# Optimization experiments

Measured on AMD Instinct MI355X. Metric: run time of the kernel, lower is better.

## Reference

```python
import jax, jax.numpy as jnp
import numpy as np

N, M, FIN, FOUT, K = 16, 65536, 32, 32, 7


def setup_inputs() -> dict:
    key = jax.random.key(0)
    k1, k2, k3, k4, k5 = jax.random.split(key, 5)
    stdv = 1.0 / np.sqrt(FIN)
    x = jax.random.normal(k1, (N, M, FIN), dtype=jnp.float32)
    weight = jax.random.uniform(k2, (K, FIN, FOUT), dtype=jnp.float32, minval=-stdv, maxval=stdv)
    bias = jax.random.uniform(k3, (FOUT,), dtype=jnp.float32, minval=-stdv, maxval=stdv)
    index_list = jax.random.randint(k4, (M * K,), 0, M, dtype=jnp.int32)
    index_value = jax.random.uniform(k5, (M, K), dtype=jnp.float32)
    return {"x": x, "weight": weight, "bias": bias,
            "index_list": index_list, "index_value": index_value}


def reference(x, weight, bias, index_list, index_value):
    # out[n,m,o] = sum_k sum_f index_value[m,k] * x[n, idx[m,k], f] * weight[k,f,o] + bias[o]
    n, m, fin = x.shape
    k = index_value.shape[1]
    idx = index_list.reshape(m, k)            # [M, K] neighbor ids
    gathered = x[:, idx, :]                    # [N, M, K, Fin] gather of neighbor feats
    weighted = gathered * index_value[None, :, :, None]  # apply adjacency weights
    out = jnp.einsum('nmkf,kfo->nmo', weighted, weight) + bias
    return out
```

## Files before the change

kernel.cpp:

```cpp
#include <hip/hip_runtime.h>
#include <hip/hip_bf16.h>

#define N_    16
#define M_    65536
#define FIN_  32
#define FOUT_ 32
#define K_    7

#define TOTAL_WAVES_ 8192
#define ITERS_       (M_ / TOTAL_WAVES_)

typedef __bf16 bf16x8 __attribute__((ext_vector_type(8)));
typedef float  f32x4  __attribute__((ext_vector_type(4)));

__global__ __launch_bounds__(256)
void transpose_kernel(const float* __restrict__ x, __bf16* __restrict__ xT)
{
    const int tid = blockIdx.x * blockDim.x + threadIdx.x;
    const int f8 = tid & 3;
    const int n  = (tid >> 2) & 15;
    const int m  = tid >> 6;

    const float4* src = (const float4*)(x + ((size_t)n * M_ + m) * FIN_ + f8 * 8);
    const float4 v0 = src[0];
    const float4 v1 = src[1];
    const float av[8] = {v0.x, v0.y, v0.z, v0.w, v1.x, v1.y, v1.z, v1.w};

    bf16x8 b;
    #pragma unroll
    for (int j = 0; j < 8; ++j) b[j] = (__bf16)av[j];

    *(bf16x8*)(xT + ((size_t)m * N_ + n) * FIN_ + f8 * 8) = b;
}

__global__ __launch_bounds__(256, 4)
void gfc_bf16_kernel(const __bf16* __restrict__ xT,
                     const float* __restrict__ w,
                     const float* __restrict__ bias,
                     const int*   __restrict__ index_list,
                     const float* __restrict__ index_value,
                     float* __restrict__ out)
{
    const int lane  = threadIdx.x & 63;
    const int col   = lane & 15;
    const int kgrp  = lane >> 4;

    const int waves_per_block = blockDim.x >> 6;
    const int wave_id = blockIdx.x * waves_per_block + (threadIdx.x >> 6);

    bf16x8 bfrag[K_][2];
    #pragma unroll
    for (int k = 0; k < K_; ++k) {
        #pragma unroll
        for (int h = 0; h < 2; ++h) {
            const float* wp = w + (size_t)k * (FIN_ * FOUT_)
                                + (size_t)(kgrp * 8) * FOUT_ + h * 16 + col;
            bf16x8 b;
            #pragma unroll
            for (int j = 0; j < 8; ++j)
                b[j] = (__bf16)wp[j * FOUT_];
            bfrag[k][h] = b;
        }
    }
    const float b_lo = bias[col];
    const float b_hi = bias[16 + col];

    const size_t lane_elt = (size_t)col * FIN_ + kgrp * 8;

    int m = __builtin_amdgcn_readfirstlane(wave_id);

    int   idxs[K_];
    float ivs[K_];
    #pragma unroll
    for (int k = 0; k < K_; ++k) {
        idxs[k] = index_list[m * K_ + k];
        ivs[k]  = index_value[m * K_ + k];
    }
    bf16x8 raw[K_];
    #pragma unroll
    for (int k = 0; k < K_; ++k)
        raw[k] = *(const bf16x8*)(xT + (size_t)idxs[k] * (N_ * FIN_) + lane_elt);

    for (int i = 0; i < ITERS_; ++i) {
        const bool has_next = (i + 1) < ITERS_;
        const int  m_next   = __builtin_amdgcn_readfirstlane(m + TOTAL_WAVES_);

        int   idxn[K_];
        float ivn[K_];
        if (has_next) {
            #pragma unroll
            for (int k = 0; k < K_; ++k) {
                idxn[k] = index_list[m_next * K_ + k];
                ivn[k]  = index_value[m_next * K_ + k];
            }
        }

        f32x4 acc0 = {0.f, 0.f, 0.f, 0.f};
        f32x4 acc1 = {0.f, 0.f, 0.f, 0.f};
        #pragma unroll
        for (int k = 0; k < K_; ++k) {
            const float ivk = ivs[k];
            bf16x8 a;
            #pragma unroll
            for (int j = 0; j < 8; ++j)
                a[j] = (__bf16)((float)raw[k][j] * ivk);
            acc0 = __builtin_amdgcn_mfma_f32_16x16x32_bf16(a, bfrag[k][0], acc0, 0, 0, 0);
            acc1 = __builtin_amdgcn_mfma_f32_16x16x32_bf16(a, bfrag[k][1], acc1, 0, 0, 0);
        }

        if (has_next) {
            #pragma unroll
            for (int k = 0; k < K_; ++k)
                raw[k] = *(const bf16x8*)(xT + (size_t)idxn[k] * (N_ * FIN_) + lane_elt);
            #pragma unroll
            for (int k = 0; k < K_; ++k) {
                idxs[k] = idxn[k];
                ivs[k]  = ivn[k];
            }
        }

        #pragma unroll
        for (int r = 0; r < 4; ++r) {
            const int n = kgrp * 4 + r;
            float* op = out + ((size_t)n * M_ + (size_t)m) * FOUT_;
            __builtin_nontemporal_store(acc0[r] + b_lo, op + col);
            __builtin_nontemporal_store(acc1[r] + b_hi, op + 16 + col);
        }

        m = m_next;
    }
}

__global__ __launch_bounds__(256, 4)
void gfc_fallback_kernel(const float* __restrict__ x,
                         const float* __restrict__ w,
                         const float* __restrict__ bias,
                         const int*   __restrict__ index_list,
                         const float* __restrict__ index_value,
                         float* __restrict__ out)
{
    const int lane  = threadIdx.x & 63;
    const int col   = lane & 15;
    const int kgrp  = lane >> 4;

    const int waves_per_block = blockDim.x >> 6;
    const int wave_id     = blockIdx.x * waves_per_block + (threadIdx.x >> 6);
    const int total_waves = gridDim.x * waves_per_block;

    bf16x8 bfrag[K_][2];
    #pragma unroll
    for (int k = 0; k < K_; ++k) {
        #pragma unroll
        for (int h = 0; h < 2; ++h) {
            const float* wp = w + (size_t)k * (FIN_ * FOUT_)
                                + (size_t)(kgrp * 8) * FOUT_ + h * 16 + col;
            bf16x8 b;
            #pragma unroll
            for (int j = 0; j < 8; ++j)
                b[j] = (__bf16)wp[j * FOUT_];
            bfrag[k][h] = b;
        }
    }
    const float b_lo = bias[col];
    const float b_hi = bias[16 + col];

    for (int m = wave_id; m < M_; m += total_waves) {
        f32x4 acc0 = {0.f, 0.f, 0.f, 0.f};
        f32x4 acc1 = {0.f, 0.f, 0.f, 0.f};

        #pragma unroll
        for (int k = 0; k < K_; ++k) {
            const int   m2  = index_list[m * K_ + k];
            const float ivk = index_value[m * K_ + k];
            const float* ap = x + ((size_t)col * M_ + (size_t)m2) * FIN_ + kgrp * 8;
            const float4 v0 = *(const float4*)(ap);
            const float4 v1 = *(const float4*)(ap + 4);
            const float av[8] = {v0.x, v0.y, v0.z, v0.w, v1.x, v1.y, v1.z, v1.w};
            bf16x8 a;
            #pragma unroll
            for (int j = 0; j < 8; ++j)
                a[j] = (__bf16)(av[j] * ivk);
            acc0 = __builtin_amdgcn_mfma_f32_16x16x32_bf16(a, bfrag[k][0], acc0, 0, 0, 0);
            acc1 = __builtin_amdgcn_mfma_f32_16x16x32_bf16(a, bfrag[k][1], acc1, 0, 0, 0);
        }

        #pragma unroll
        for (int r = 0; r < 4; ++r) {
            const int n = kgrp * 4 + r;
            const size_t base = ((size_t)n * M_ + (size_t)m) * FOUT_;
            out[base + col]      = acc0[r] + b_lo;
            out[base + 16 + col] = acc1[r] + b_hi;
        }
    }
}

extern "C" void kernel_launch(void* const* d_in, const int* in_sizes, int n_in,
                              void* d_out, int out_size, void* d_ws, size_t ws_size,
                              hipStream_t stream) {
    const float* x    = (const float*)d_in[0];
    const float* w    = (const float*)d_in[1];
    const float* bias = (const float*)d_in[2];
    const int*   il   = (const int*)  d_in[3];
    const float* iv   = (const float*)d_in[4];
    float* out = (float*)d_out;

    const size_t ws_needed = (size_t)M_ * N_ * FIN_ * sizeof(__bf16);
    if (ws_size >= ws_needed) {
        __bf16* xT = (__bf16*)d_ws;
        const int t_total = N_ * M_ * FIN_ / 8;
        hipLaunchKernelGGL(transpose_kernel, dim3(t_total / 256), dim3(256), 0, stream,
                           x, xT);
        hipLaunchKernelGGL(gfc_bf16_kernel, dim3(2048), dim3(256), 0, stream,
                           xT, w, bias, il, iv, out);
    } else {
        hipLaunchKernelGGL(gfc_fallback_kernel, dim3(2048), dim3(256), 0, stream,
                           x, w, bias, il, iv, out);
    }
}
```

Baseline: 311.2 us.

## Partition batch across XCDs so each die's L2 holds its own bf16 slice

Drops the [M,N,FIN] transpose and writes x as plain bf16 in its original [N,M,FIN] layout. The main kernel is remapped so each XCD (blockIdx & 7) handles only two batch slices, and each MFMA row is now one of 16 consecutive m values rather than one of 16 n values. The per-XCD gather working set therefore fits in that XCD's L2, and the convert kernel becomes a straight streaming copy. Weight fragments move from registers into LDS to cut register pressure, at the cost of per-k LDS reads and more scattered index loads per lane.

Measured after the change: 340.6 us. +9.4%, slower.

```diff
diff --git a/kernel.cpp b/kernel.cpp
--- a/kernel.cpp
+++ b/kernel.cpp
@@ -7,91 +7,97 @@
 #define FOUT_ 32
 #define K_    7
 
-#define TOTAL_WAVES_ 8192
-#define ITERS_       (M_ / TOTAL_WAVES_)
+#define BLOCKS_   2048
+#define THREADS_  256
+#define WAVES_PB_ 4
+#define NXCD_     8
+#define WAVES_PER_XCD_ ((BLOCKS_ / NXCD_) * WAVES_PB_)
+#define GROUPS_   (M_ / 16)
+#define ITERS_    8
 
 typedef __bf16 bf16x8 __attribute__((ext_vector_type(8)));
 typedef float  f32x4  __attribute__((ext_vector_type(4)));
 
 __global__ __launch_bounds__(256)
-void transpose_kernel(const float* __restrict__ x, __bf16* __restrict__ xT)
+void convert_kernel(const float* __restrict__ x, __bf16* __restrict__ xb)
 {
-    const int tid = blockIdx.x * blockDim.x + threadIdx.x;
-    const int f8 = tid & 3;
-    const int n  = (tid >> 2) & 15;
-    const int m  = tid >> 6;
-
-    const float4* src = (const float4*)(x + ((size_t)n * M_ + m) * FIN_ + f8 * 8);
-    const float4 v0 = src[0];
-    const float4 v1 = src[1];
-    const float av[8] = {v0.x, v0.y, v0.z, v0.w, v1.x, v1.y, v1.z, v1.w};
-
+    const size_t tid = (size_t)blockIdx.x * blockDim.x + threadIdx.x;
+    const f32x4* src = (const f32x4*)x + tid * 2;
+    const f32x4 v0 = __builtin_nontemporal_load(src);
+    const f32x4 v1 = __builtin_nontemporal_load(src + 1);
     bf16x8 b;
     #pragma unroll
-    for (int j = 0; j < 8; ++j) b[j] = (__bf16)av[j];
-
-    *(bf16x8*)(xT + ((size_t)m * N_ + n) * FIN_ + f8 * 8) = b;
+    for (int j = 0; j < 4; ++j) b[j] = (__bf16)v0[j];
+    #pragma unroll
+    for (int j = 0; j < 4; ++j) b[4 + j] = (__bf16)v1[j];
+    *(bf16x8*)(xb + tid * 8) = b;
 }
 
 __global__ __launch_bounds__(256, 4)
-void gfc_bf16_kernel(const __bf16* __restrict__ xT,
-                     const float* __restrict__ w,
-                     const float* __restrict__ bias,
-                     const int*   __restrict__ index_list,
-                     const float* __restrict__ index_value,
-                     float* __restrict__ out)
+void gfc_xcd_kernel(const __bf16* __restrict__ xb,
+                    const float* __restrict__ w,
+                    const float* __restrict__ bias,
+                    const int*   __restrict__ il,
+                    const float* __restrict__ iv,
+                    float* __restrict__ out)
 {
-    const int lane  = threadIdx.x & 63;
-    const int col   = lane & 15;
-    const int kgrp  = lane >> 4;
-
-    const int waves_per_block = blockDim.x >> 6;
-    const int wave_id = blockIdx.x * waves_per_block + (threadIdx.x >> 6);
-
-    bf16x8 bfrag[K_][2];
-    #pragma unroll
-    for (int k = 0; k < K_; ++k) {
-        #pragma unroll
-        for (int h = 0; h < 2; ++h) {
-            const float* wp = w + (size_t)k * (FIN_ * FOUT_)
-                                + (size_t)(kgrp * 8) * FOUT_ + h * 16 + col;
-            bf16x8 b;
-            #pragma unroll
-            for (int j = 0; j < 8; ++j)
-                b[j] = (__bf16)wp[j * FOUT_];
-            bfrag[k][h] = b;
-        }
-    }
+    __shared__ __bf16 wlds[K_ * 2 * 64 * 8];
+
+    const int lane = threadIdx.x & 63;
+    const int col  = lane & 15;
+    const int kgrp = lane >> 4;
+
+    for (int t = threadIdx.x; t < K_ * 2 * 64; t += THREADS_) {
+        const int l  = t & 63;
+        const int h  = (t >> 6) & 1;
+        const int k  = t >> 7;
+        const int c  = l & 15;
+        const int kg = l >> 4;
+        const float* wp = w + (size_t)k * (FIN_ * FOUT_)
+                            + (size_t)(kg * 8) * FOUT_ + h * 16 + c;
+        bf16x8 b;
+        #pragma unroll
+        for (int j = 0; j < 8; ++j) b[j] = (__bf16)wp[j * FOUT_];
+        *(bf16x8*)(wlds + (size_t)t * 8) = b;
+    }
+    __syncthreads();
+
     const float b_lo = bias[col];
     const float b_hi = bias[16 + col];
 
-    const size_t lane_elt = (size_t)col * FIN_ + kgrp * 8;
-
-    int m = __builtin_amdgcn_readfirstlane(wave_id);
+    const int xcd  = blockIdx.x & (NXCD_ - 1);
+    const int widx = (blockIdx.x >> 3) * WAVES_PB_ + (threadIdx.x >> 6);
 
     int   idxs[K_];
     float ivs[K_];
-    #pragma unroll
-    for (int k = 0; k < K_; ++k) {
-        idxs[k] = index_list[m * K_ + k];
-        ivs[k]  = index_value[m * K_ + k];
+    {
+        const int m0 = (widx * 4) * 16 + col;
+        #pragma unroll
+        for (int k = 0; k < K_; ++k) {
+            idxs[k] = il[m0 * K_ + k];
+            ivs[k]  = iv[m0 * K_ + k];
+        }
     }
     bf16x8 raw[K_];
-    #pragma unroll
-    for (int k = 0; k < K_; ++k)
-        raw[k] = *(const bf16x8*)(xT + (size_t)idxs[k] * (N_ * FIN_) + lane_elt);
-
-    for (int i = 0; i < ITERS_; ++i) {
-        const bool has_next = (i + 1) < ITERS_;
-        const int  m_next   = __builtin_amdgcn_readfirstlane(m + TOTAL_WAVES_);
+    {
+        const __bf16* xn = xb + (size_t)(xcd * 2) * (M_ * FIN_);
+        #pragma unroll
+        for (int k = 0; k < K_; ++k)
+            raw[k] = *(const bf16x8*)(xn + (size_t)idxs[k] * FIN_ + kgrp * 8);
+    }
+
+    for (int it = 0; it < ITERS_; ++it) {
+        const bool has_next = (it + 1) < ITERS_;
 
         int   idxn[K_];
         float ivn[K_];
         if (has_next) {
+            const int it2 = it + 1;
+            const int mn  = (widx * 4 + (it2 & 3)) * 16 + col;
             #pragma unroll
             for (int k = 0; k < K_; ++k) {
-                idxn[k] = index_list[m_next * K_ + k];
-                ivn[k]  = index_value[m_next * K_ + k];
+                idxn[k] = il[mn * K_ + k];
+                ivn[k]  = iv[mn * K_ + k];
             }
         }
 
@@ -104,30 +110,31 @@
             #pragma unroll
             for (int j = 0; j < 8; ++j)
                 a[j] = (__bf16)((float)raw[k][j] * ivk);
-            acc0 = __builtin_amdgcn_mfma_f32_16x16x32_bf16(a, bfrag[k][0], acc0, 0, 0, 0);
-            acc1 = __builtin_amdgcn_mfma_f32_16x16x32_bf16(a, bfrag[k][1], acc1, 0, 0, 0);
+            const bf16x8 bf0 = *(const bf16x8*)(wlds + ((k * 2 + 0) * 64 + lane) * 8);
+            const bf16x8 bf1 = *(const bf16x8*)(wlds + ((k * 2 + 1) * 64 + lane) * 8);
+            acc0 = __builtin_amdgcn_mfma_f32_16x16x32_bf16(a, bf0, acc0, 0, 0, 0);
+            acc1 = __builtin_amdgcn_mfma_f32_16x16x32_bf16(a, bf1, acc1, 0, 0, 0);
         }
 
         if (has_next) {
+            const int it2 = it + 1;
+            const int nn  = xcd * 2 + (it2 >> 2);
+            const __bf16* xn = xb + (size_t)nn * (M_ * FIN_);
             #pragma unroll
             for (int k = 0; k < K_; ++k)
-                raw[k] = *(const bf16x8*)(xT + (size_t)idxn[k] * (N_ * FIN_) + lane_elt);
-            #pragma unroll
-            for (int k = 0; k < K_; ++k) {
-                idxs[k] = idxn[k];
-                ivs[k]  = ivn[k];
-            }
-        }
-
+                raw[k] = *(const bf16x8*)(xn + (size_t)idxn[k] * FIN_ + kgrp * 8);
+            #pragma unroll
+            for (int k = 0; k < K_; ++k) { idxs[k] = idxn[k]; ivs[k] = ivn[k]; }
+        }
+
+        const int n_cur = xcd * 2 + (it >> 2);
+        const int mb    = (widx * 4 + (it & 3)) * 16;
         #pragma unroll
         for (int r = 0; r < 4; ++r) {
-            const int n = kgrp * 4 + r;
-            float* op = out + ((size_t)n * M_ + (size_t)m) * FOUT_;
+            float* op = out + ((size_t)n_cur * M_ + (size_t)(mb + kgrp * 4 + r)) * FOUT_;
             __builtin_nontemporal_store(acc0[r] + b_lo, op + col);
             __builtin_nontemporal_store(acc1[r] + b_hi, op + 16 + col);
         }
-
-        m = m_next;
     }
 }
 
@@ -206,12 +213,12 @@
 
     const size_t ws_needed = (size_t)M_ * N_ * FIN_ * sizeof(__bf16);
     if (ws_size >= ws_needed) {
-        __bf16* xT = (__bf16*)d_ws;
+        __bf16* xb = (__bf16*)d_ws;
         const int t_total = N_ * M_ * FIN_ / 8;
-        hipLaunchKernelGGL(transpose_kernel, dim3(t_total / 256), dim3(256), 0, stream,
-                           x, xT);
-        hipLaunchKernelGGL(gfc_bf16_kernel, dim3(2048), dim3(256), 0, stream,
-                           xT, w, bias, il, iv, out);
+        hipLaunchKernelGGL(convert_kernel, dim3(t_total / 256), dim3(256), 0, stream,
+                           x, xb);
+        hipLaunchKernelGGL(gfc_xcd_kernel, dim3(BLOCKS_), dim3(THREADS_), 0, stream,
+                           xb, w, bias, il, iv, out);
     } else {
         hipLaunchKernelGGL(gfc_fallback_kernel, dim3(2048), dim3(256), 0, stream,
                            x, w, bias, il, iv, out);
```
